# Kernel optimization log

Hardware: AMD Instinct MI355X
Metric: run time of the kernel (lower is better)

Reference implementation:

```python
import jax, jax.numpy as jnp
import numpy as np

N = 50000
E = 800000
F_IN = 128
HID = 64
HEADS = 4
P = 16384


def setup_inputs() -> dict:
    key = jax.random.key(0)
    ks = jax.random.split(key, 20)
    s = 0.05
    inp = {
        'x': jax.random.normal(ks[0], (N, F_IN), jnp.float32),
        'edge_src': jax.random.randint(ks[1], (E,), 0, N, jnp.int32),
        'edge_dst': jax.random.randint(ks[2], (E,), 0, N, jnp.int32),
        'edge_attr': jax.random.uniform(ks[3], (E, 1), jnp.float32),
        'pair_indices': jax.random.randint(ks[4], (P, 2), 0, N, jnp.int32),
        # conv1: in=F_IN, heads=4, out=HID, edge_dim=1
        'W1': jax.random.normal(ks[5], (F_IN, HEADS * HID), jnp.float32) * s,
        'We1': jax.random.normal(ks[6], (1, HEADS * HID), jnp.float32) * s,
        'as1': jax.random.normal(ks[7], (HEADS, HID), jnp.float32) * s,
        'ad1': jax.random.normal(ks[8], (HEADS, HID), jnp.float32) * s,
        'ae1': jax.random.normal(ks[9], (HEADS, HID), jnp.float32) * s,
        'b1': jnp.zeros((HEADS * HID,), jnp.float32),
        # conv2: in=4*HID, heads=1, out=HID
        'W2': jax.random.normal(ks[10], (HEADS * HID, HID), jnp.float32) * s,
        'We2': jax.random.normal(ks[11], (1, HID), jnp.float32) * s,
        'as2': jax.random.normal(ks[12], (1, HID), jnp.float32) * s,
        'ad2': jax.random.normal(ks[13], (1, HID), jnp.float32) * s,
        'ae2': jax.random.normal(ks[14], (1, HID), jnp.float32) * s,
        'b2': jnp.zeros((HID,), jnp.float32),
        'Wlin': jax.random.normal(ks[15], (2 * HID, 1), jnp.float32) * s,
        'blin': jnp.zeros((1,), jnp.float32),
    }
    return inp


def gat_conv(x, src, dst, edge_attr, W, We, att_src, att_dst, att_edge, bias, heads, C):
    """PyG GATConv (add_self_loops=True, fill_value='mean', negative_slope=0.2, eval mode)."""
    n = x.shape[0]
    # self-loop edge_attr = mean of incoming edge attrs per node
    deg = jax.ops.segment_sum(jnp.ones_like(dst, dtype=edge_attr.dtype), dst, num_segments=n)
    loop_attr = jax.ops.segment_sum(edge_attr, dst, num_segments=n) / jnp.maximum(deg, 1.0)[:, None]
    loop = jnp.arange(n, dtype=src.dtype)
    src_f = jnp.concatenate([src, loop])
    dst_f = jnp.concatenate([dst, loop])
    ea = jnp.concatenate([edge_attr, loop_attr], axis=0)  # [E+N, 1]
    h = (x @ W).reshape(n, heads, C)                      # [N, H, C]
    a_src = (h * att_src).sum(-1)                         # [N, H]
    a_dst = (h * att_dst).sum(-1)
    e = (ea @ We).reshape(-1, heads, C)                   # [E+N, H, C]
    a_edge = (e * att_edge).sum(-1)                       # [E+N, H]
    alpha = jax.nn.leaky_relu(a_src[src_f] + a_dst[dst_f] + a_edge, 0.2)
    amax = jax.ops.segment_max(alpha, dst_f, num_segments=n)
    ex = jnp.exp(alpha - amax[dst_f])
    denom = jax.ops.segment_sum(ex, dst_f, num_segments=n)
    w = ex / denom[dst_f]                                 # segment softmax over dst
    msg = h[src_f] * w[..., None]                         # [E+N, H, C]
    out = jax.ops.segment_sum(msg, dst_f, num_segments=n) # [N, H, C]
    return out.reshape(n, heads * C) + bias


def reference(x, edge_src, edge_dst, edge_attr, pair_indices,
              W1, We1, as1, ad1, ae1, b1,
              W2, We2, as2, ad2, ae2, b2, Wlin, blin):
    # dropout is identity in eval mode
    h1 = jax.nn.elu(gat_conv(x, edge_src, edge_dst, edge_attr,
                             W1, We1, as1, ad1, ae1, b1, HEADS, HID))
    h2 = gat_conv(h1, edge_src, edge_dst, edge_attr,
                  W2, We2, as2, ad2, ae2, b2, 1, HID)
    d1 = h2[pair_indices[:, 0]]
    d2 = h2[pair_indices[:, 1]]
    pf = jnp.concatenate([d1, d2], axis=1)                # [P, 2*HID]
    return jax.nn.sigmoid(pf @ Wlin + blin).reshape(-1)
```

## Files before the change

kernel.cpp:

```cpp
#include <hip/hip_runtime.h>
#include <hip/hip_fp16.h>
#include <math.h>

typedef __attribute__((ext_vector_type(8))) short short8;
typedef __attribute__((ext_vector_type(4))) float floatx4;
typedef __attribute__((ext_vector_type(2))) float float2v;

__device__ __forceinline__ unsigned short f2bf(float f){
  unsigned int x = __float_as_uint(f);
  unsigned int r = x + 0x7fff + ((x >> 16) & 1);
  return (unsigned short)(r >> 16);
}
__device__ __forceinline__ unsigned char f2fp8(float v){
  int pk = __builtin_amdgcn_cvt_pk_fp8_f32(v, 0.f, 0, false);
  return (unsigned char)(pk & 0xff);
}
__device__ __forceinline__ float wsumf(float v){
#pragma unroll
  for (int o = 32; o; o >>= 1) v += __shfl_xor(v, o, 64);
  return v;
}

__global__ __launch_bounds__(256) void k_count(const int* __restrict__ dst,
    const float* __restrict__ eattr, unsigned long long* __restrict__ degp,
    int* __restrict__ rank, int E, int Eq, int N){
  int e = blockIdx.x * 256 + threadIdx.x;
  if (e >= E) return;
  int d = dst[e];
  float ea = eattr[e];
  int b = (e >= Eq) + (e >= 2 * Eq) + (e >= 3 * Eq);
  unsigned long long add = (1ull << 40) |
      (unsigned long long)(ea * 16777216.0f);
  unsigned long long old = atomicAdd(&degp[(size_t)b * N + d], add);
  rank[e] = (int)(old >> 40);
}

__global__ __launch_bounds__(256) void k_scan1(const unsigned long long* __restrict__ degp,
    int* __restrict__ row_ptr, int* __restrict__ bsum, int n){
  __shared__ int sm[2][256];
  int tid = threadIdx.x, gid = blockIdx.x * 256 + tid;
  int v = 0;
  if (gid < n){
#pragma unroll
    for (int b = 0; b < 4; b++) v += (int)(degp[(size_t)b * n + gid] >> 40);
  }
  sm[0][tid] = v; __syncthreads();
  int pin = 0;
  for (int off = 1; off < 256; off <<= 1){
    int t = sm[pin][tid];
    if (tid >= off) t += sm[pin][tid - off];
    sm[pin ^ 1][tid] = t; pin ^= 1; __syncthreads();
  }
  int incl = sm[pin][tid];
  if (gid < n) row_ptr[gid] = incl - v;
  if (tid == 255) bsum[blockIdx.x] = incl;
}

__global__ __launch_bounds__(256) void k_scan2(const int* __restrict__ bsum,
    int* __restrict__ bofs, int nb){
  __shared__ int sm[2][256];
  int tid = threadIdx.x;
  int v = (tid < nb) ? bsum[tid] : 0;
  sm[0][tid] = v; __syncthreads();
  int pin = 0;
  for (int off = 1; off < 256; off <<= 1){
    int t = sm[pin][tid];
    if (tid >= off) t += sm[pin][tid - off];
    sm[pin ^ 1][tid] = t; pin ^= 1; __syncthreads();
  }
  bofs[tid] = sm[pin][tid] - v;
}

__global__ __launch_bounds__(256) void k_scan3(int* __restrict__ row_ptr,
    const int* __restrict__ bofs, const unsigned long long* __restrict__ degp,
    float* __restrict__ lattr, int4* __restrict__ nodeinfo, int n, int E){
  int gid = blockIdx.x * 256 + threadIdx.x;
  if (gid >= n) return;
  int rp = row_ptr[gid] + bofs[gid >> 8];
  row_ptr[gid] = rp;
  const unsigned long long M40 = (1ull << 40) - 1;
  unsigned long long p0 = degp[gid];
  unsigned long long p1 = degp[(size_t)n + gid];
  unsigned long long p2 = degp[(size_t)2 * n + gid];
  unsigned long long p3 = degp[(size_t)3 * n + gid];
  int d0 = (int)(p0 >> 40), d1 = (int)(p1 >> 40), d2 = (int)(p2 >> 40), d3 = (int)(p3 >> 40);
  float dtot = (float)(d0 + d1 + d2 + d3);
  float s = ((float)(p0 & M40) + (float)(p1 & M40) + (float)(p2 & M40) + (float)(p3 & M40))
            * (1.0f / 16777216.0f);
  lattr[gid] = s / fmaxf(dtot, 1.0f);
  nodeinfo[gid] = make_int4(rp, d0, d0 + d1, d0 + d1 + d2);
  if (gid == 0) row_ptr[n] = E;
}

__global__ __launch_bounds__(256) void k_scatter(const int* __restrict__ src,
    const int* __restrict__ dst, const float* __restrict__ eattr,
    const int* __restrict__ rank, const int4* __restrict__ nodeinfo,
    int2* __restrict__ csr, int E, int Eq){
  int e = blockIdx.x * 256 + threadIdx.x;
  if (e >= E) return;
  int d = dst[e];
  int4 ni = nodeinfo[d];
  int b = (e >= Eq) + (e >= 2 * Eq) + (e >= 3 * Eq);
  int cum = b == 0 ? 0 : b == 1 ? ni.y : b == 2 ? ni.z : ni.w;
  int pos = ni.x + cum + rank[e];
  csr[pos] = make_int2(src[e], __float_as_int(eattr[e]));
}

__global__ void k_prep(const float* __restrict__ W1, const float* __restrict__ as1,
    const float* __restrict__ ad1, const float* __restrict__ W2,
    const float* __restrict__ as2, const float* __restrict__ ad2,
    const float* __restrict__ We1, const float* __restrict__ ae1,
    const float* __restrict__ We2, const float* __restrict__ ae2,
    unsigned short* __restrict__ W1p, unsigned short* __restrict__ W2p,
    float* __restrict__ ce){
  int b = blockIdx.x, lane = threadIdx.x;
  if (b < 68){
    int nt = b >> 2, kc = b & 3;
    int col = lane & 15, krow = kc * 32 + (lane >> 4) * 8;
    unsigned short tmp[8];
    if (nt < 16){
#pragma unroll
      for (int j = 0; j < 8; j++) tmp[j] = f2bf(W1[(size_t)(krow + j) * 256 + nt * 16 + col]);
    } else {
#pragma unroll
      for (int j = 0; j < 8; j++){
        float v = 0.f;
        if (col < 8){
          const float* av = (col < 4) ? as1 : ad1;
          int h = col & 3;
          for (int c = 0; c < 64; c++)
            v += W1[(size_t)(krow + j) * 256 + h * 64 + c] * av[h * 64 + c];
        }
        tmp[j] = f2bf(v);
      }
    }
    unsigned short* dstp = W1p + (((size_t)nt * 4 + kc) * 64 + lane) * 8;
    *(ushort4*)(dstp)     = make_ushort4(tmp[0], tmp[1], tmp[2], tmp[3]);
    *(ushort4*)(dstp + 4) = make_ushort4(tmp[4], tmp[5], tmp[6], tmp[7]);
  } else if (b < 108){
    int bb = b - 68;
    int nt = bb >> 3, kc = bb & 7;
    int col = lane & 15, krow = kc * 32 + (lane >> 4) * 8;
    unsigned short tmp[8];
    if (nt < 4){
#pragma unroll
      for (int j = 0; j < 8; j++) tmp[j] = f2bf(W2[(size_t)(krow + j) * 64 + nt * 16 + col]);
    } else {
#pragma unroll
      for (int j = 0; j < 8; j++){
        float v = 0.f;
        if (col < 2){
          const float* av = (col == 0) ? as2 : ad2;
          for (int c = 0; c < 64; c++)
            v += W2[(size_t)(krow + j) * 64 + c] * av[c];
        }
        tmp[j] = f2bf(v);
      }
    }
    unsigned short* dstp = W2p + (((size_t)nt * 8 + kc) * 64 + lane) * 8;
    *(ushort4*)(dstp)     = make_ushort4(tmp[0], tmp[1], tmp[2], tmp[3]);
    *(ushort4*)(dstp + 4) = make_ushort4(tmp[4], tmp[5], tmp[6], tmp[7]);
  } else {
    float p0 = We1[lane]       * ae1[lane];
    float p1 = We1[64 + lane]  * ae1[64 + lane];
    float p2 = We1[128 + lane] * ae1[128 + lane];
    float p3 = We1[192 + lane] * ae1[192 + lane];
    float p4 = We2[lane]       * ae2[lane];
    p0 = wsumf(p0); p1 = wsumf(p1); p2 = wsumf(p2); p3 = wsumf(p3); p4 = wsumf(p4);
    if (lane == 0){ ce[0] = p0; ce[1] = p1; ce[2] = p2; ce[3] = p3; ce[4] = p4; }
  }
}

__global__ __launch_bounds__(256) void k_gemm1_att(const float* __restrict__ A,
    const unsigned short* __restrict__ Bp, unsigned char* __restrict__ h1f8,
    float* __restrict__ asrc, float* __restrict__ adst, int M){
  constexpr int K = 128, NKC = 4;
  __shared__ unsigned short Bs[256 * K];
  {
    const uint4* srcp = (const uint4*)Bp;
    uint4* dstp = (uint4*)Bs;
    for (int i = threadIdx.x; i < 4096; i += 256) dstp[i] = srcp[i];
  }
  __syncthreads();
  int wave = threadIdx.x >> 6, lane = threadIdx.x & 63;
  int quad = lane >> 4, col = lane & 15;
  int r0 = (blockIdx.x * 4 + wave) * 16;
  int rowc = min(r0 + col, M - 1);
  short8 af[NKC], sf[NKC];
#pragma unroll
  for (int kc = 0; kc < NKC; kc++){
    float4 a0 = *(const float4*)(A + (size_t)rowc * K + kc * 32 + quad * 8);
    float4 a1 = *(const float4*)(A + (size_t)rowc * K + kc * 32 + quad * 8 + 4);
    short8 t;
    t[0] = (short)f2bf(a0.x); t[1] = (short)f2bf(a0.y);
    t[2] = (short)f2bf(a0.z); t[3] = (short)f2bf(a0.w);
    t[4] = (short)f2bf(a1.x); t[5] = (short)f2bf(a1.y);
    t[6] = (short)f2bf(a1.z); t[7] = (short)f2bf(a1.w);
    af[kc] = t;
    sf[kc] = *(const short8*)(Bp + (((size_t)16 * 4 + kc) * 64 + lane) * 8);
  }
  floatx4 acc[17];
#pragma unroll
  for (int nt = 0; nt < 17; nt++) acc[nt] = (floatx4){0.f, 0.f, 0.f, 0.f};
#pragma unroll
  for (int kc = 0; kc < NKC; kc++){
#pragma unroll
    for (int nt = 0; nt < 16; nt++){
      short8 bfv = *(const short8*)(&Bs[((nt * NKC + kc) * 64 + lane) * 8]);
      acc[nt] = __builtin_amdgcn_mfma_f32_16x16x32_bf16(af[kc], bfv, acc[nt], 0, 0, 0);
    }
    acc[16] = __builtin_amdgcn_mfma_f32_16x16x32_bf16(af[kc], sf[kc], acc[16], 0, 0, 0);
  }
#pragma unroll
  for (int nt = 0; nt < 16; nt++){
#pragma unroll
    for (int i = 0; i < 4; i++){
      int r = r0 + quad * 4 + i;
      if (r < M) h1f8[(size_t)r * 256 + nt * 16 + col] = f2fp8(acc[nt][i]);
    }
  }
#pragma unroll
  for (int i = 0; i < 4; i++){
    int r = r0 + quad * 4 + i;
    if (r < M){
      float v = acc[16][i];
      if (col < 4)      asrc[(size_t)r * 4 + col] = v;
      else if (col < 8) adst[(size_t)r * 4 + (col - 4)] = v;
    }
  }
}

__global__ __launch_bounds__(256) void k_gemm2_att(const unsigned short* __restrict__ A,
    const unsigned short* __restrict__ Bp, unsigned char* __restrict__ h2f8,
    float* __restrict__ asrc, float* __restrict__ adst, int M){
  constexpr int K = 256, NKC = 8;
  __shared__ unsigned short Bs[64 * K];
  {
    const uint4* srcp = (const uint4*)Bp;
    uint4* dstp = (uint4*)Bs;
    for (int i = threadIdx.x; i < 2048; i += 256) dstp[i] = srcp[i];
  }
  __syncthreads();
  int wave = threadIdx.x >> 6, lane = threadIdx.x & 63;
  int quad = lane >> 4, col = lane & 15;
  int r0 = (blockIdx.x * 4 + wave) * 16;
  int rowc = min(r0 + col, M - 1);
  short8 af[NKC], sf[NKC];
#pragma unroll
  for (int kc = 0; kc < NKC; kc++){
    af[kc] = *(const short8*)(A + (size_t)rowc * K + kc * 32 + quad * 8);
    sf[kc] = *(const short8*)(Bp + (((size_t)4 * 8 + kc) * 64 + lane) * 8);
  }
  floatx4 acc[5];
#pragma unroll
  for (int nt = 0; nt < 5; nt++) acc[nt] = (floatx4){0.f, 0.f, 0.f, 0.f};
#pragma unroll
  for (int kc = 0; kc < NKC; kc++){
#pragma unroll
    for (int nt = 0; nt < 4; nt++){
      short8 bfv = *(const short8*)(&Bs[((nt * NKC + kc) * 64 + lane) * 8]);
      acc[nt] = __builtin_amdgcn_mfma_f32_16x16x32_bf16(af[kc], bfv, acc[nt], 0, 0, 0);
    }
    acc[4] = __builtin_amdgcn_mfma_f32_16x16x32_bf16(af[kc], sf[kc], acc[4], 0, 0, 0);
  }
#pragma unroll
  for (int nt = 0; nt < 4; nt++){
#pragma unroll
    for (int i = 0; i < 4; i++){
      int r = r0 + quad * 4 + i;
      if (r < M) h2f8[(size_t)r * 64 + nt * 16 + col] = f2fp8(acc[nt][i]);
    }
  }
#pragma unroll
  for (int i = 0; i < 4; i++){
    int r = r0 + quad * 4 + i;
    if (r < M){
      float v = acc[4][i];
      if (col == 0)      asrc[r] = v;
      else if (col == 1) adst[r] = v;
    }
  }
}

__global__ __launch_bounds__(256) void k_gat1(
    const int* __restrict__ row_ptr, const int2* __restrict__ csr,
    const float* __restrict__ lattr,
    const float* __restrict__ a_src, const float* __restrict__ a_dst,
    const float* __restrict__ ce, const unsigned char* __restrict__ hpre,
    const float* __restrict__ bias, unsigned short* __restrict__ hout, int n){
  int node = blockIdx.x * 4 + (threadIdx.x >> 6);
  if (node >= n) return;
  int lane = threadIdx.x & 63;
  int q = lane >> 4, lsub = lane & 15, hq = lsub >> 2;
  int start = row_ptr[node], deg = row_ptr[node + 1] - start;
  int total = deg + 1;
  float4 as4 = *(const float4*)(a_src + (size_t)node * 4);
  float4 ad4 = *(const float4*)(a_dst + (size_t)node * 4);
  float4 ce4 = *(const float4*)ce;
  float la = lattr[node];
  float asvh = hq == 0 ? as4.x : hq == 1 ? as4.y : hq == 2 ? as4.z : as4.w;
  float advh = hq == 0 ? ad4.x : hq == 1 ? ad4.y : hq == 2 ? ad4.z : ad4.w;
  float ceh  = hq == 0 ? ce4.x : hq == 1 ? ce4.y : hq == 2 ? ce4.z : ce4.w;
  float aself = asvh + advh + la * ceh;
  aself = aself > 0.f ? aself : 0.2f * aself;
  float wself = __expf(aself);
  float2v acc2[8];
#pragma unroll
  for (int k = 0; k < 8; k++) acc2[k] = (float2v){0.f, 0.f};
  float dn = 0.f;
  for (int e = q; e < total; e += 4){
    int s; float wv;
    if (e < deg){
      int2 se = csr[start + e];
      s = se.x;
      float ea = __int_as_float(se.y);
      float a = a_src[(size_t)s * 4 + hq] + advh + ea * ceh;
      a = a > 0.f ? a : 0.2f * a;
      wv = __expf(a);
    } else { s = node; wv = wself; }
    dn += wv;
    uint4 u = *(const uint4*)(hpre + (size_t)s * 256 + lsub * 16);
    float2v w2 = (float2v){wv, wv};
    unsigned uu[4] = {u.x, u.y, u.z, u.w};
#pragma unroll
    for (int j = 0; j < 4; j++){
      float2v lo = __builtin_amdgcn_cvt_pk_f32_fp8((int)uu[j], false);
      float2v hi = __builtin_amdgcn_cvt_pk_f32_fp8((int)uu[j], true);
      acc2[2 * j]     += w2 * lo;
      acc2[2 * j + 1] += w2 * hi;
    }
  }
  dn += __shfl_xor(dn, 16, 64);
  dn += __shfl_xor(dn, 32, 64);
#pragma unroll
  for (int k = 0; k < 8; k++){
    acc2[k].x += __shfl_xor(acc2[k].x, 16, 64);
    acc2[k].x += __shfl_xor(acc2[k].x, 32, 64);
    acc2[k].y += __shfl_xor(acc2[k].y, 16, 64);
    acc2[k].y += __shfl_xor(acc2[k].y, 32, 64);
  }
  if (q == 0){
    float inv = 1.f / dn;
    float bb[16];
#pragma unroll
    for (int j = 0; j < 4; j++){
      float4 b4 = *(const float4*)(bias + lsub * 16 + j * 4);
      bb[j * 4 + 0] = b4.x; bb[j * 4 + 1] = b4.y;
      bb[j * 4 + 2] = b4.z; bb[j * 4 + 3] = b4.w;
    }
    unsigned short o[16];
#pragma unroll
    for (int k = 0; k < 16; k++){
      float av = (k & 1) ? acc2[k >> 1].y : acc2[k >> 1].x;
      float v = av * inv + bb[k];
      v = v > 0.f ? v : (__expf(v) - 1.f);
      o[k] = f2bf(v);
    }
    unsigned short* op = hout + (size_t)node * 256 + lsub * 16;
    *(uint4*)(op)     = *(uint4*)(o);
    *(uint4*)(op + 8) = *(uint4*)(o + 8);
  }
}

__global__ __launch_bounds__(256) void k_gat2(
    const int* __restrict__ row_ptr, const int2* __restrict__ csr,
    const float* __restrict__ lattr,
    const float* __restrict__ a_src, const float* __restrict__ a_dst,
    const float* __restrict__ ce, const unsigned char* __restrict__ hpre,
    const float* __restrict__ bias, const float* __restrict__ Wlin,
    float* __restrict__ s1v, float* __restrict__ s2v, int n){
  int node = blockIdx.x * 4 + (threadIdx.x >> 6);
  if (node >= n) return;
  int lane = threadIdx.x & 63;
  int slot = lane >> 3, lsub = lane & 7;
  int start = row_ptr[node], deg = row_ptr[node + 1] - start;
  int total = deg + 1;
  float adn = a_dst[node], c = ce[4];
  float aself = a_src[node] + adn + lattr[node] * c;
  aself = aself > 0.f ? aself : 0.2f * aself;
  float wself = __expf(aself);
  float2v acc2[4];
#pragma unroll
  for (int k = 0; k < 4; k++) acc2[k] = (float2v){0.f, 0.f};
  float dn = 0.f;
  for (int e = slot; e < total; e += 8){
    int s; float wv;
    if (e < deg){
      int2 se = csr[start + e];
      s = se.x;
      float ea = __int_as_float(se.y);
      float a = a_src[s] + adn + ea * c;
      a = a > 0.f ? a : 0.2f * a;
      wv = __expf(a);
    } else { s = node; wv = wself; }
    dn += wv;
    uint2 u = *(const uint2*)(hpre + (size_t)s * 64 + lsub * 8);
    float2v w2 = (float2v){wv, wv};
    unsigned uu[2] = {u.x, u.y};
#pragma unroll
    for (int j = 0; j < 2; j++){
      float2v lo = __builtin_amdgcn_cvt_pk_f32_fp8((int)uu[j], false);
      float2v hi = __builtin_amdgcn_cvt_pk_f32_fp8((int)uu[j], true);
      acc2[2 * j]     += w2 * lo;
      acc2[2 * j + 1] += w2 * hi;
    }
  }
#pragma unroll
  for (int o = 8; o < 64; o <<= 1){
    dn += __shfl_xor(dn, o, 64);
#pragma unroll
    for (int k = 0; k < 4; k++){
      acc2[k].x += __shfl_xor(acc2[k].x, o, 64);
      acc2[k].y += __shfl_xor(acc2[k].y, o, 64);
    }
  }
  float inv = 1.f / dn;
  float t1 = 0.f, t2 = 0.f;
#pragma unroll
  for (int k = 0; k < 8; k++){
    float av = (k & 1) ? acc2[k >> 1].y : acc2[k >> 1].x;
    float v = av * inv + bias[lsub * 8 + k];
    t1 += v * Wlin[lsub * 8 + k];
    t2 += v * Wlin[64 + lsub * 8 + k];
  }
#pragma unroll
  for (int o = 1; o < 8; o <<= 1){
    t1 += __shfl_xor(t1, o, 64);
    t2 += __shfl_xor(t2, o, 64);
  }
  if (lane == 0){ s1v[node] = t1; s2v[node] = t2; }
}

__global__ __launch_bounds__(256) void k_pairs(const int* __restrict__ pairs,
    const float* __restrict__ s1v, const float* __restrict__ s2v,
    const float* __restrict__ blin, float* __restrict__ out, int P){
  int p = blockIdx.x * 256 + threadIdx.x;
  if (p >= P) return;
  int i = pairs[2 * p], j = pairs[2 * p + 1];
  float x = s1v[i] + s2v[j] + blin[0];
  out[p] = 1.f / (1.f + __expf(-x));
}

extern "C" void kernel_launch(void* const* d_in, const int* in_sizes, int n_in,
                              void* d_out, int out_size, void* d_ws, size_t ws_size,
                              hipStream_t stream) {
  const float* x     = (const float*)d_in[0];
  const int*   esrc  = (const int*)  d_in[1];
  const int*   edst  = (const int*)  d_in[2];
  const float* eattr = (const float*)d_in[3];
  const int*   pairs = (const int*)  d_in[4];
  const float* W1    = (const float*)d_in[5];
  const float* We1   = (const float*)d_in[6];
  const float* as1   = (const float*)d_in[7];
  const float* ad1   = (const float*)d_in[8];
  const float* ae1   = (const float*)d_in[9];
  const float* b1    = (const float*)d_in[10];
  const float* W2    = (const float*)d_in[11];
  const float* We2   = (const float*)d_in[12];
  const float* as2   = (const float*)d_in[13];
  const float* ad2   = (const float*)d_in[14];
  const float* ae2   = (const float*)d_in[15];
  const float* b2    = (const float*)d_in[16];
  const float* Wlin  = (const float*)d_in[17];
  const float* blin  = (const float*)d_in[18];
  float* out = (float*)d_out;

  const int N = in_sizes[0] / 128;
  const int E = in_sizes[1];
  const int Eq = (E + 3) / 4;
  const int P = in_sizes[4] / 2;

  char* w = (char*)d_ws;
  size_t off = 0;
  auto alloc = [&](size_t bytes) -> size_t {
    size_t r = off; off = (off + bytes + 255) & ~(size_t)255; return r;
  };
  size_t o_degp   = alloc((size_t)N * 32);
  size_t zero_end = off;
  size_t o_rank   = alloc((size_t)E * 4);
  size_t o_rowptr = alloc((size_t)(N + 1) * 4);
  size_t o_bsum   = alloc(1024);
  size_t o_bofs   = alloc(1024);
  size_t o_lattr  = alloc((size_t)N * 4);
  size_t o_ninfo  = alloc((size_t)N * 16);
  size_t o_csr    = alloc((size_t)E * 8);
  size_t o_asrc1  = alloc((size_t)N * 16);
  size_t o_adst1  = alloc((size_t)N * 16);
  size_t o_asrc2  = alloc((size_t)N * 4);
  size_t o_adst2  = alloc((size_t)N * 4);
  size_t o_ce     = alloc(32);
  size_t o_s1     = alloc((size_t)N * 4);
  size_t o_s2     = alloc((size_t)N * 4);
  size_t o_W1p    = alloc((size_t)17 * 4 * 64 * 8 * 2);
  size_t o_W2p    = alloc((size_t)5 * 8 * 64 * 8 * 2);
  size_t o_h1f8   = alloc((size_t)N * 256);
  size_t o_h1b    = alloc((size_t)N * 256 * 2);
  size_t o_h2f8   = alloc((size_t)N * 64);
  (void)ws_size;

  unsigned long long* degp = (unsigned long long*)(w + o_degp);
  int*   rank   = (int*)  (w + o_rank);
  int*   rowptr = (int*)  (w + o_rowptr);
  int*   bsum   = (int*)  (w + o_bsum);
  int*   bofs   = (int*)  (w + o_bofs);
  float* lattr  = (float*)(w + o_lattr);
  int4*  ninfo  = (int4*) (w + o_ninfo);
  int2*  csr    = (int2*) (w + o_csr);
  float* asrc1  = (float*)(w + o_asrc1);
  float* adst1  = (float*)(w + o_adst1);
  float* asrc2  = (float*)(w + o_asrc2);
  float* adst2  = (float*)(w + o_adst2);
  float* ce     = (float*)(w + o_ce);
  float* s1v    = (float*)(w + o_s1);
  float* s2v    = (float*)(w + o_s2);
  unsigned short* W1p = (unsigned short*)(w + o_W1p);
  unsigned short* W2p = (unsigned short*)(w + o_W2p);
  unsigned char*  h1f8 = (unsigned char*)(w + o_h1f8);
  unsigned short* h1b  = (unsigned short*)(w + o_h1b);
  unsigned char*  h2f8 = (unsigned char*)(w + o_h2f8);

  hipMemsetAsync(w, 0, zero_end, stream);

  int ebl = (E + 255) / 256;
  int nbl = (N + 255) / 256;
  int wbl = (N + 3) / 4;

  k_count<<<ebl, 256, 0, stream>>>(edst, eattr, degp, rank, E, Eq, N);
  k_scan1<<<nbl, 256, 0, stream>>>(degp, rowptr, bsum, N);
  k_scan2<<<1, 256, 0, stream>>>(bsum, bofs, nbl);
  k_scan3<<<nbl, 256, 0, stream>>>(rowptr, bofs, degp, lattr, ninfo, N, E);
  k_scatter<<<ebl, 256, 0, stream>>>(esrc, edst, eattr, rank, ninfo, csr, E, Eq);

  k_prep<<<109, 64, 0, stream>>>(W1, as1, ad1, W2, as2, ad2,
                                 We1, ae1, We2, ae2, W1p, W2p, ce);

  k_gemm1_att<<<(N + 63) / 64, 256, 0, stream>>>(x, W1p, h1f8, asrc1, adst1, N);
  k_gat1<<<wbl, 256, 0, stream>>>(rowptr, csr, lattr, asrc1, adst1, ce,
                                  h1f8, b1, h1b, N);
  k_gemm2_att<<<(N + 63) / 64, 256, 0, stream>>>(h1b, W2p, h2f8, asrc2, adst2, N);
  k_gat2<<<wbl, 256, 0, stream>>>(rowptr, csr, lattr, asrc2, adst2, ce,
                                  h2f8, b2, Wlin, s1v, s2v, N);
  k_pairs<<<(P + 255) / 256, 256, 0, stream>>>(pairs, s1v, s2v, blin, out, P);
}
```

Baseline: 292.9 us.

## Use 8 interleaved atomic bins for CSR build and unroll GAT edge loops

The degree-count atomics are spread over 8 bins chosen by block index (interleaved) instead of 4 contiguous edge quarters. The scan now writes a per-node 8-entry base-offset table, so the scatter does a single lookup. Both GAT aggregation kernels handle the self-loop separately and process two edges per iteration, issuing two independent gathers to raise memory-level parallelism. In exchange the degree buffer and base table double in size, scan3 reads 8 bins per node, and the edge order within each CSR row changes, which can shift floating-point summation order.

```diff
diff --git a/kernel.cpp b/kernel.cpp
--- a/kernel.cpp
+++ b/kernel.cpp
@@ -23,14 +23,13 @@
 
 __global__ __launch_bounds__(256) void k_count(const int* __restrict__ dst,
     const float* __restrict__ eattr, unsigned long long* __restrict__ degp,
-    int* __restrict__ rank, int E, int Eq, int N){
+    int* __restrict__ rank, int E, int N){
   int e = blockIdx.x * 256 + threadIdx.x;
   if (e >= E) return;
+  int b = blockIdx.x & 7;
   int d = dst[e];
-  float ea = eattr[e];
-  int b = (e >= Eq) + (e >= 2 * Eq) + (e >= 3 * Eq);
   unsigned long long add = (1ull << 40) |
-      (unsigned long long)(ea * 16777216.0f);
+      (unsigned long long)(eattr[e] * 16777216.0f);
   unsigned long long old = atomicAdd(&degp[(size_t)b * N + d], add);
   rank[e] = (int)(old >> 40);
 }
@@ -42,7 +41,7 @@
   int v = 0;
   if (gid < n){
 #pragma unroll
-    for (int b = 0; b < 4; b++) v += (int)(degp[(size_t)b * n + gid] >> 40);
+    for (int b = 0; b < 8; b++) v += (int)(degp[(size_t)b * n + gid] >> 40);
   }
   sm[0][tid] = v; __syncthreads();
   int pin = 0;
@@ -73,36 +72,37 @@
 
 __global__ __launch_bounds__(256) void k_scan3(int* __restrict__ row_ptr,
     const int* __restrict__ bofs, const unsigned long long* __restrict__ degp,
-    float* __restrict__ lattr, int4* __restrict__ nodeinfo, int n, int E){
+    float* __restrict__ lattr, int* __restrict__ base, int n, int E){
   int gid = blockIdx.x * 256 + threadIdx.x;
   if (gid >= n) return;
   int rp = row_ptr[gid] + bofs[gid >> 8];
   row_ptr[gid] = rp;
   const unsigned long long M40 = (1ull << 40) - 1;
-  unsigned long long p0 = degp[gid];
-  unsigned long long p1 = degp[(size_t)n + gid];
-  unsigned long long p2 = degp[(size_t)2 * n + gid];
-  unsigned long long p3 = degp[(size_t)3 * n + gid];
-  int d0 = (int)(p0 >> 40), d1 = (int)(p1 >> 40), d2 = (int)(p2 >> 40), d3 = (int)(p3 >> 40);
-  float dtot = (float)(d0 + d1 + d2 + d3);
-  float s = ((float)(p0 & M40) + (float)(p1 & M40) + (float)(p2 & M40) + (float)(p3 & M40))
-            * (1.0f / 16777216.0f);
-  lattr[gid] = s / fmaxf(dtot, 1.0f);
-  nodeinfo[gid] = make_int4(rp, d0, d0 + d1, d0 + d1 + d2);
+  int cum = 0; float s = 0.f;
+  int bb[8];
+#pragma unroll
+  for (int b = 0; b < 8; b++){
+    unsigned long long p = degp[(size_t)b * n + gid];
+    bb[b] = rp + cum;
+    cum += (int)(p >> 40);
+    s += (float)(p & M40);
+  }
+  lattr[gid] = (s * (1.0f / 16777216.0f)) / fmaxf((float)cum, 1.0f);
+  int4* bp = (int4*)(base + (size_t)gid * 8);
+  bp[0] = make_int4(bb[0], bb[1], bb[2], bb[3]);
+  bp[1] = make_int4(bb[4], bb[5], bb[6], bb[7]);
   if (gid == 0) row_ptr[n] = E;
 }
 
 __global__ __launch_bounds__(256) void k_scatter(const int* __restrict__ src,
     const int* __restrict__ dst, const float* __restrict__ eattr,
-    const int* __restrict__ rank, const int4* __restrict__ nodeinfo,
-    int2* __restrict__ csr, int E, int Eq){
+    const int* __restrict__ rank, const int* __restrict__ base,
+    int2* __restrict__ csr, int E){
   int e = blockIdx.x * 256 + threadIdx.x;
   if (e >= E) return;
+  int b = blockIdx.x & 7;
   int d = dst[e];
-  int4 ni = nodeinfo[d];
-  int b = (e >= Eq) + (e >= 2 * Eq) + (e >= 3 * Eq);
-  int cum = b == 0 ? 0 : b == 1 ? ni.y : b == 2 ? ni.z : ni.w;
-  int pos = ni.x + cum + rank[e];
+  int pos = base[(size_t)d * 8 + b] + rank[e];
   csr[pos] = make_int2(src[e], __float_as_int(eattr[e]));
 }
 
@@ -293,7 +293,6 @@
   int lane = threadIdx.x & 63;
   int q = lane >> 4, lsub = lane & 15, hq = lsub >> 2;
   int start = row_ptr[node], deg = row_ptr[node + 1] - start;
-  int total = deg + 1;
   float4 as4 = *(const float4*)(a_src + (size_t)node * 4);
   float4 ad4 = *(const float4*)(a_dst + (size_t)node * 4);
   float4 ce4 = *(const float4*)ce;
@@ -301,33 +300,46 @@
   float asvh = hq == 0 ? as4.x : hq == 1 ? as4.y : hq == 2 ? as4.z : as4.w;
   float advh = hq == 0 ? ad4.x : hq == 1 ? ad4.y : hq == 2 ? ad4.z : ad4.w;
   float ceh  = hq == 0 ? ce4.x : hq == 1 ? ce4.y : hq == 2 ? ce4.z : ce4.w;
-  float aself = asvh + advh + la * ceh;
-  aself = aself > 0.f ? aself : 0.2f * aself;
-  float wself = __expf(aself);
   float2v acc2[8];
 #pragma unroll
   for (int k = 0; k < 8; k++) acc2[k] = (float2v){0.f, 0.f};
   float dn = 0.f;
-  for (int e = q; e < total; e += 4){
-    int s; float wv;
-    if (e < deg){
-      int2 se = csr[start + e];
-      s = se.x;
-      float ea = __int_as_float(se.y);
-      float a = a_src[(size_t)s * 4 + hq] + advh + ea * ceh;
-      a = a > 0.f ? a : 0.2f * a;
-      wv = __expf(a);
-    } else { s = node; wv = wself; }
-    dn += wv;
-    uint4 u = *(const uint4*)(hpre + (size_t)s * 256 + lsub * 16);
-    float2v w2 = (float2v){wv, wv};
+  if (q == 0){
+    float aself = asvh + advh + la * ceh;
+    aself = aself > 0.f ? aself : 0.2f * aself;
+    float wself = __expf(aself);
+    dn = wself;
+    uint4 u = *(const uint4*)(hpre + (size_t)node * 256 + lsub * 16);
+    float2v w2 = (float2v){wself, wself};
     unsigned uu[4] = {u.x, u.y, u.z, u.w};
 #pragma unroll
     for (int j = 0; j < 4; j++){
-      float2v lo = __builtin_amdgcn_cvt_pk_f32_fp8((int)uu[j], false);
-      float2v hi = __builtin_amdgcn_cvt_pk_f32_fp8((int)uu[j], true);
-      acc2[2 * j]     += w2 * lo;
-      acc2[2 * j + 1] += w2 * hi;
+      acc2[2 * j]     = w2 * __builtin_amdgcn_cvt_pk_f32_fp8((int)uu[j], false);
+      acc2[2 * j + 1] = w2 * __builtin_amdgcn_cvt_pk_f32_fp8((int)uu[j], true);
+    }
+  }
+  for (int e = q; e < deg; e += 8){
+    bool vB = (e + 4) < deg;
+    int2 seA = csr[start + e];
+    int2 seB = csr[start + (vB ? e + 4 : e)];
+    float aA = a_src[(size_t)seA.x * 4 + hq] + advh + __int_as_float(seA.y) * ceh;
+    aA = aA > 0.f ? aA : 0.2f * aA;
+    float wA = __expf(aA);
+    float aB = a_src[(size_t)seB.x * 4 + hq] + advh + __int_as_float(seB.y) * ceh;
+    aB = aB > 0.f ? aB : 0.2f * aB;
+    float wB = vB ? __expf(aB) : 0.f;
+    uint4 uA = *(const uint4*)(hpre + (size_t)seA.x * 256 + lsub * 16);
+    uint4 uB = *(const uint4*)(hpre + (size_t)seB.x * 256 + lsub * 16);
+    dn += wA + wB;
+    float2v wA2 = (float2v){wA, wA}, wB2 = (float2v){wB, wB};
+    unsigned ua[4] = {uA.x, uA.y, uA.z, uA.w};
+    unsigned ub[4] = {uB.x, uB.y, uB.z, uB.w};
+#pragma unroll
+    for (int j = 0; j < 4; j++){
+      acc2[2 * j]     += wA2 * __builtin_amdgcn_cvt_pk_f32_fp8((int)ua[j], false);
+      acc2[2 * j + 1] += wA2 * __builtin_amdgcn_cvt_pk_f32_fp8((int)ua[j], true);
+      acc2[2 * j]     += wB2 * __builtin_amdgcn_cvt_pk_f32_fp8((int)ub[j], false);
+      acc2[2 * j + 1] += wB2 * __builtin_amdgcn_cvt_pk_f32_fp8((int)ub[j], true);
     }
   }
   dn += __shfl_xor(dn, 16, 64);
@@ -374,35 +386,47 @@
   int lane = threadIdx.x & 63;
   int slot = lane >> 3, lsub = lane & 7;
   int start = row_ptr[node], deg = row_ptr[node + 1] - start;
-  int total = deg + 1;
   float adn = a_dst[node], c = ce[4];
-  float aself = a_src[node] + adn + lattr[node] * c;
-  aself = aself > 0.f ? aself : 0.2f * aself;
-  float wself = __expf(aself);
   float2v acc2[4];
 #pragma unroll
   for (int k = 0; k < 4; k++) acc2[k] = (float2v){0.f, 0.f};
   float dn = 0.f;
-  for (int e = slot; e < total; e += 8){
-    int s; float wv;
-    if (e < deg){
-      int2 se = csr[start + e];
-      s = se.x;
-      float ea = __int_as_float(se.y);
-      float a = a_src[s] + adn + ea * c;
-      a = a > 0.f ? a : 0.2f * a;
-      wv = __expf(a);
-    } else { s = node; wv = wself; }
-    dn += wv;
-    uint2 u = *(const uint2*)(hpre + (size_t)s * 64 + lsub * 8);
-    float2v w2 = (float2v){wv, wv};
+  if (slot == 0){
+    float aself = a_src[node] + adn + lattr[node] * c;
+    aself = aself > 0.f ? aself : 0.2f * aself;
+    float wself = __expf(aself);
+    dn = wself;
+    uint2 u = *(const uint2*)(hpre + (size_t)node * 64 + lsub * 8);
+    float2v w2 = (float2v){wself, wself};
     unsigned uu[2] = {u.x, u.y};
 #pragma unroll
     for (int j = 0; j < 2; j++){
-      float2v lo = __builtin_amdgcn_cvt_pk_f32_fp8((int)uu[j], false);
-      float2v hi = __builtin_amdgcn_cvt_pk_f32_fp8((int)uu[j], true);
-      acc2[2 * j]     += w2 * lo;
-      acc2[2 * j + 1] += w2 * hi;
+      acc2[2 * j]     = w2 * __builtin_amdgcn_cvt_pk_f32_fp8((int)uu[j], false);
+      acc2[2 * j + 1] = w2 * __builtin_amdgcn_cvt_pk_f32_fp8((int)uu[j], true);
+    }
+  }
+  for (int e = slot; e < deg; e += 16){
+    bool vB = (e + 8) < deg;
+    int2 seA = csr[start + e];
+    int2 seB = csr[start + (vB ? e + 8 : e)];
+    float aA = a_src[seA.x] + adn + __int_as_float(seA.y) * c;
+    aA = aA > 0.f ? aA : 0.2f * aA;
+    float wA = __expf(aA);
+    float aB = a_src[seB.x] + adn + __int_as_float(seB.y) * c;
+    aB = aB > 0.f ? aB : 0.2f * aB;
+    float wB = vB ? __expf(aB) : 0.f;
+    uint2 uA = *(const uint2*)(hpre + (size_t)seA.x * 64 + lsub * 8);
+    uint2 uB = *(const uint2*)(hpre + (size_t)seB.x * 64 + lsub * 8);
+    dn += wA + wB;
+    float2v wA2 = (float2v){wA, wA}, wB2 = (float2v){wB, wB};
+    unsigned ua[2] = {uA.x, uA.y};
+    unsigned ub[2] = {uB.x, uB.y};
+#pragma unroll
+    for (int j = 0; j < 2; j++){
+      acc2[2 * j]     += wA2 * __builtin_amdgcn_cvt_pk_f32_fp8((int)ua[j], false);
+      acc2[2 * j + 1] += wA2 * __builtin_amdgcn_cvt_pk_f32_fp8((int)ua[j], true);
+      acc2[2 * j]     += wB2 * __builtin_amdgcn_cvt_pk_f32_fp8((int)ub[j], false);
+      acc2[2 * j + 1] += wB2 * __builtin_amdgcn_cvt_pk_f32_fp8((int)ub[j], true);
     }
   }
 #pragma unroll
@@ -467,7 +491,6 @@
 
   const int N = in_sizes[0] / 128;
   const int E = in_sizes[1];
-  const int Eq = (E + 3) / 4;
   const int P = in_sizes[4] / 2;
 
   char* w = (char*)d_ws;
@@ -475,14 +498,14 @@
   auto alloc = [&](size_t bytes) -> size_t {
     size_t r = off; off = (off + bytes + 255) & ~(size_t)255; return r;
   };
-  size_t o_degp   = alloc((size_t)N * 32);
+  size_t o_degp   = alloc((size_t)N * 64);
   size_t zero_end = off;
   size_t o_rank   = alloc((size_t)E * 4);
   size_t o_rowptr = alloc((size_t)(N + 1) * 4);
   size_t o_bsum   = alloc(1024);
   size_t o_bofs   = alloc(1024);
   size_t o_lattr  = alloc((size_t)N * 4);
-  size_t o_ninfo  = alloc((size_t)N * 16);
+  size_t o_base   = alloc((size_t)N * 32);
   size_t o_csr    = alloc((size_t)E * 8);
   size_t o_asrc1  = alloc((size_t)N * 16);
   size_t o_adst1  = alloc((size_t)N * 16);
@@ -504,7 +527,7 @@
   int*   bsum   = (int*)  (w + o_bsum);
   int*   bofs   = (int*)  (w + o_bofs);
   float* lattr  = (float*)(w + o_lattr);
-  int4*  ninfo  = (int4*) (w + o_ninfo);
+  int*   base   = (int*)  (w + o_base);
   int2*  csr    = (int2*) (w + o_csr);
   float* asrc1  = (float*)(w + o_asrc1);
   float* adst1  = (float*)(w + o_adst1);
@@ -525,11 +548,11 @@
   int nbl = (N + 255) / 256;
   int wbl = (N + 3) / 4;
 
-  k_count<<<ebl, 256, 0, stream>>>(edst, eattr, degp, rank, E, Eq, N);
+  k_count<<<ebl, 256, 0, stream>>>(edst, eattr, degp, rank, E, N);
   k_scan1<<<nbl, 256, 0, stream>>>(degp, rowptr, bsum, N);
   k_scan2<<<1, 256, 0, stream>>>(bsum, bofs, nbl);
-  k_scan3<<<nbl, 256, 0, stream>>>(rowptr, bofs, degp, lattr, ninfo, N, E);
-  k_scatter<<<ebl, 256, 0, stream>>>(esrc, edst, eattr, rank, ninfo, csr, E, Eq);
+  k_scan3<<<nbl, 256, 0, stream>>>(rowptr, bofs, degp, lattr, base, N, E);
+  k_scatter<<<ebl, 256, 0, stream>>>(esrc, edst, eattr, rank, base, csr, E);
 
   k_prep<<<109, 64, 0, stream>>>(W1, as1, ad1, W2, as2, ad2,
                                  We1, ae1, We2, ae2, W1p, W2p, ce);
```

After: 280.2 us. 1.05x faster.
